# Optimization experiments

Hardware: AMD Instinct MI355X
Metric: run time of the kernel (lower is better)

## Reference

```python
import jax, jax.numpy as jnp
import numpy as np

T, N, D = 64, 40, 4
H, R, K = 256, 64, 2
E = N * (N - 1)


def _xavier(key, shape):
    std = (2.0 / (shape[0] + shape[1])) ** 0.5
    return (std * jax.random.normal(key, shape)).astype(jnp.float32)


def setup_inputs() -> dict:
    ks = iter(jax.random.split(jax.random.key(0), 40))
    send, recv = np.where(np.ones((N, N)) - np.eye(N))  # fully-connected directed graph, E = N*(N-1)
    p = {}
    p['inputs'] = jax.random.normal(next(ks), (1, T, N, D), dtype=jnp.float32)
    p['node_masks'] = jnp.ones((1, T, N), dtype=jnp.float32)
    p['send_edges'] = jnp.asarray(send, dtype=jnp.int32)
    p['recv_edges'] = jnp.asarray(recv, dtype=jnp.int32)
    for name, nin in (('mlp1', D), ('mlp2', 2 * H), ('mlp3', H), ('mlp4', 3 * H)):
        p[name + '_W1'] = _xavier(next(ks), (H, nin))
        p[name + '_b1'] = jnp.full((H,), 0.1, jnp.float32)
        p[name + '_W2'] = _xavier(next(ks), (H, H))
        p[name + '_b2'] = jnp.full((H,), 0.1, jnp.float32)
    s = float(1.0 / np.sqrt(R))
    for nm in ('fwd', 'rev'):
        p[nm + '_Wih'] = jax.random.uniform(next(ks), (4 * R, H), jnp.float32, -s, s)
        p[nm + '_Whh'] = jax.random.uniform(next(ks), (4 * R, R), jnp.float32, -s, s)
        p[nm + '_bih'] = jnp.zeros((4 * R,), jnp.float32)
        p[nm + '_bhh'] = jnp.zeros((4 * R,), jnp.float32)
    p['enc_W'] = _xavier(next(ks), (K, 2 * R))
    p['enc_b'] = jnp.full((K,), 0.1, jnp.float32)
    p['prior_W'] = _xavier(next(ks), (K, R))
    p['prior_b'] = jnp.full((K,), 0.1, jnp.float32)
    return p


def _mlp(x, W1, b1, W2, b2):
    # RefNRIMLP in eval mode with no_bn=True: elu(fc2(elu(fc1(x))))
    return jax.nn.elu(jax.nn.elu(x @ W1.T + b1) @ W2.T + b2)


def _lstm(xs, Wih, Whh, bih, bhh):
    # xs: [T, E, H] -> hidden states [T, E, R]; PyTorch LSTM gate order i, f, g, o
    def step(carry, xt):
        h, c = carry
        g = xt @ Wih.T + bih + h @ Whh.T + bhh
        i, f, gg, o = jnp.split(g, 4, axis=-1)
        c = jax.nn.sigmoid(f) * c + jax.nn.sigmoid(i) * jnp.tanh(gg)
        h = jax.nn.sigmoid(o) * jnp.tanh(c)
        return (h, c), h
    Rh = Whh.shape[1]
    init = (jnp.zeros((xs.shape[1], Rh), xs.dtype), jnp.zeros((xs.shape[1], Rh), xs.dtype))
    _, hs = jax.lax.scan(step, init, xs)
    return hs


def _encode(inputs, send, recv,
            m1W1, m1b1, m1W2, m1b2, m2W1, m2b1, m2W2, m2b2,
            m3W1, m3b1, m3W2, m3b2, m4W1, m4b1, m4W2, m4b2,
            fWih, fWhh, fbih, fbhh, rWih, rWhh, rbih, rbhh,
            encW, encb, priW, prib):
    x = inputs[0]                                                  # [T, N, D]
    h = _mlp(x, m1W1, m1b1, m1W2, m1b2)                            # [T, N, H]
    e = jnp.concatenate([h[:, send], h[:, recv]], axis=-1)         # node2edge gather [T, E, 2H]
    e = _mlp(e, m2W1, m2b1, m2W2, m2b2)                            # [T, E, H]
    skip = e
    n = jnp.zeros((x.shape[0], x.shape[1], e.shape[-1]), e.dtype)
    n = n.at[:, recv].add(e)                                       # edge2node scatter-add (index_add_)
    n = _mlp(n, m3W1, m3b1, m3W2, m3b2)                            # [T, N, H]
    e = jnp.concatenate([n[:, send], n[:, recv], skip], axis=-1)   # [T, E, 3H]
    e = _mlp(e, m4W1, m4b1, m4W2, m4b2)                            # per-edge features over time [T, E, H]
    fwd_h = _lstm(e, fWih, fWhh, fbih, fbhh)                       # [T, E, R]
    rev_h = _lstm(e[::-1], rWih, rWhh, rbih, rbhh)[::-1]           # [T, E, R]
    prior = fwd_h @ priW.T + prib                                  # [T, E, K]
    enc = jnp.concatenate([fwd_h, rev_h], axis=-1) @ encW.T + encb # [T, E, K]
    return jnp.concatenate([prior, enc], axis=-1)                  # [T, E, 2K]


def reference(inputs, node_masks, send_edges, recv_edges,
              mlp1_W1, mlp1_b1, mlp1_W2, mlp1_b2,
              mlp2_W1, mlp2_b1, mlp2_W2, mlp2_b2,
              mlp3_W1, mlp3_b1, mlp3_W2, mlp3_b2,
              mlp4_W1, mlp4_b1, mlp4_W2, mlp4_b2,
              fwd_Wih, fwd_Whh, fwd_bih, fwd_bhh,
              rev_Wih, rev_Whh, rev_bih, rev_bhh,
              enc_W, enc_b, prior_W, prior_b):
    del node_masks  # all nodes present -> static fully-connected graph each step
    return _encode(inputs, send_edges, recv_edges,
                   mlp1_W1, mlp1_b1, mlp1_W2, mlp1_b2,
                   mlp2_W1, mlp2_b1, mlp2_W2, mlp2_b2,
                   mlp3_W1, mlp3_b1, mlp3_W2, mlp3_b2,
                   mlp4_W1, mlp4_b1, mlp4_W2, mlp4_b2,
                   fwd_Wih, fwd_Whh, fwd_bih, fwd_bhh,
                   rev_Wih, rev_Whh, rev_bih, rev_bhh,
                   enc_W, enc_b, prior_W, prior_b)
```

## Files before the change

### kernel.cpp

```cpp
#include <hip/hip_runtime.h>
#include <math.h>

#define T_ 64
#define N_ 40
#define D_ 4
#define H_ 256
#define R_ 64
#define E_ 1560
#define TE_ (T_*E_)
#define TN_ (T_*N_)

typedef unsigned short us;
typedef short short8 __attribute__((ext_vector_type(8)));
typedef float f32x4 __attribute__((ext_vector_type(4)));

__device__ __forceinline__ float elu_f(float x){ return x > 0.f ? x : (__expf(x) - 1.f); }
__device__ __forceinline__ float sig_f(float x){ return 1.f/(1.f+__expf(-x)); }
__device__ __forceinline__ float tanh_f(float x){ return 2.f/(1.f+__expf(-2.f*x)) - 1.f; }
__device__ __forceinline__ float dot4(float4 a, float4 b){ return a.x*b.x + a.y*b.y + a.z*b.z + a.w*b.w; }

__device__ __forceinline__ float bf2f(us u){ return __uint_as_float(((unsigned int)u) << 16); }
__device__ __forceinline__ us f2bf(float f){
    unsigned int u = __float_as_uint(f);
    u += 0x7FFFu + ((u >> 16) & 1u);
    return (us)(u >> 16);
}
__device__ __forceinline__ float4 ld4f(const float* p){ return *(const float4*)p; }
__device__ __forceinline__ float4 ld4f(const us* p){
    ushort4 v = *(const ushort4*)p;
    return make_float4(bf2f(v.x), bf2f(v.y), bf2f(v.z), bf2f(v.w));
}
__device__ __forceinline__ void st4f(float* p, float4 v){ *(float4*)p = v; }
__device__ __forceinline__ void st4f(us* p, float4 v){
    ushort4 o; o.x = f2bf(v.x); o.y = f2bf(v.y); o.z = f2bf(v.z); o.w = f2bf(v.w);
    *(ushort4*)p = o;
}

__device__ __forceinline__ void gld16(void* lds, const void* g){
    __builtin_amdgcn_global_load_lds((const __attribute__((address_space(1))) unsigned int*)g,
                                     (__attribute__((address_space(3))) unsigned int*)lds,
                                     16, 0, 0);
}

__device__ __forceinline__ void wsplit1(const float* W, us* hi, us* lo, int i){
    const float w = W[i];
    const us h = f2bf(w);
    hi[i] = h;
    lo[i] = f2bf(w - bf2f(h));
}

__device__ __forceinline__ void wsplitF(const float* __restrict__ W, int stride, int colOff,
                                        us* hi, us* lo, int i){
    const int jj   = i & 7;
    const int lane = (i >> 3) & 63;
    const int mt   = (i >> 9) & 1;
    const int k    = (i >> 10) & 7;
    const int fh   = i >> 13;
    const int R = fh * 32 + mt * 16 + (lane & 15);
    const int K = k * 32 + (lane >> 4) * 8 + jj;
    const float w = W[(size_t)R * stride + colOff + K];
    const us h = f2bf(w);
    hi[i] = h;
    lo[i] = f2bf(w - bf2f(h));
}

__global__ __launch_bounds__(256)
void wsplit_all(const float* __restrict__ s0, us* h0, us* l0,
                const float* __restrict__ s1, us* h1, us* l1,
                const float* __restrict__ s2, us* h2, us* l2,
                const float* __restrict__ s3, us* h3, us* l3,
                const float* __restrict__ s4, us* h4, us* l4,
                const float* __restrict__ s5, us* h5, us* l5,
                const float* __restrict__ s6, us* h6, us* l6)
{
    int i = blockIdx.x * 256 + threadIdx.x;
    if (i < 65536) { wsplitF(s0, 256,   0, h0, l0, i); return; } i -= 65536;
    if (i < 65536) { wsplitF(s1, 768, 512, h1, l1, i); return; } i -= 65536;
    if (i < 65536) { wsplitF(s2, 256,   0, h2, l2, i); return; } i -= 65536;
    if (i < 65536) { wsplitF(s3, 256,   0, h3, l3, i); return; } i -= 65536;
    if (i < 65536) { wsplitF(s4, 256,   0, h4, l4, i); return; } i -= 65536;
    if (i < 16384) { wsplit1(s5, h5, l5, i); return; } i -= 16384;
    wsplit1(s6, h6, l6, i);
}

__global__ __launch_bounds__(256)
void mlp1_kernel(const float* __restrict__ x,
                 const float* __restrict__ W1, const float* __restrict__ b1,
                 const float* __restrict__ W2, const float* __restrict__ b2,
                 us* __restrict__ hout)
{
    __shared__ float xs[8][4];
    __shared__ float h1[8][256];
    const int tid = threadIdx.x;
    const int r0  = blockIdx.x * 8;

    if (tid < 32) xs[tid >> 2][tid & 3] = x[r0 * 4 + tid];
    __syncthreads();

    const float4 w1 = *(const float4*)&W1[tid * 4];
    const float bb1 = b1[tid];
    #pragma unroll
    for (int row = 0; row < 8; ++row) {
        float v = bb1 + xs[row][0]*w1.x + xs[row][1]*w1.y + xs[row][2]*w1.z + xs[row][3]*w1.w;
        h1[row][tid] = elu_f(v);
    }
    __syncthreads();

    float acc[8];
    const float bb2 = b2[tid];
    #pragma unroll
    for (int row = 0; row < 8; ++row) acc[row] = bb2;
    const float* w2row = W2 + (size_t)tid * 256;
    for (int k4 = 0; k4 < 64; ++k4) {
        const float4 w = *(const float4*)&w2row[k4 * 4];
        #pragma unroll
        for (int row = 0; row < 8; ++row) {
            const float4 hh = *(const float4*)&h1[row][k4 * 4];
            acc[row] += dot4(hh, w);
        }
    }
    #pragma unroll
    for (int row = 0; row < 8; ++row)
        hout[(size_t)(r0 + row) * 256 + tid] = f2bf(elu_f(acc[row]));
}

__global__ __launch_bounds__(256)
void node_proj(const us* __restrict__ A, const float* __restrict__ W,
               int wstride, float* __restrict__ P)
{
    __shared__ float As[16][64];
    __shared__ float Ws[16][64];

    const int tid  = threadIdx.x;
    const int am   = tid >> 2;
    const int gm   = blockIdx.x * 64 + am;
    const int part = blockIdx.y >> 2;
    const int wq   = blockIdx.y & 3;

    const us* aptr = A + (size_t)gm * 256;
    const float* wptr = W + (size_t)(wq * 64 + am) * wstride + part * 256;

    const int tx = tid & 15, ty = tid >> 4;
    float acc[4][4] = {};

    for (int k0 = 0; k0 < 256; k0 += 16) {
        const float4 a4 = ld4f(aptr + k0 + (tid & 3) * 4);
        const float4 w4 = *(const float4*)(wptr + k0 + (tid & 3) * 4);

        __syncthreads();
        const int ak = (tid & 3) * 4;
        As[ak+0][am] = a4.x; As[ak+1][am] = a4.y; As[ak+2][am] = a4.z; As[ak+3][am] = a4.w;
        Ws[ak+0][am] = w4.x; Ws[ak+1][am] = w4.y; Ws[ak+2][am] = w4.z; Ws[ak+3][am] = w4.w;
        __syncthreads();

        #pragma unroll
        for (int kq = 0; kq < 16; ++kq) {
            const float4 av = *(const float4*)&As[kq][ty * 4];
            const float4 wv = *(const float4*)&Ws[kq][tx * 4];
            const float a_[4] = {av.x, av.y, av.z, av.w};
            const float w_[4] = {wv.x, wv.y, wv.z, wv.w};
            #pragma unroll
            for (int i = 0; i < 4; ++i)
                #pragma unroll
                for (int j = 0; j < 4; ++j)
                    acc[i][j] += a_[i] * w_[j];
        }
    }

    const int gn = part * 256 + wq * 64 + tx * 4;
    #pragma unroll
    for (int i = 0; i < 4; ++i) {
        const int row = blockIdx.x * 64 + ty * 4 + i;
        float4 o;
        o.x = acc[i][0]; o.y = acc[i][1]; o.z = acc[i][2]; o.w = acc[i][3];
        *(float4*)(P + (size_t)row * 512 + gn) = o;
    }
}

#define VM0   0x3F70

#define GEMM_CORE64(WHp, WLp)                                                            \
    {                                                                                    \
        const us* wbh = (WHp) + w * 8192 + lane * 8;                                     \
        const us* wbl = (WLp) + w * 8192 + lane * 8;                                     \
        _Pragma("unroll")                                                                \
        for (int k = 0; k < 8; ++k) {                                                    \
            short8 wh[2], wl[2], ef[4];                                                  \
            _Pragma("unroll")                                                            \
            for (int mt = 0; mt < 2; ++mt) {                                             \
                wh[mt] = *(const short8*)(wbh + (k * 2 + mt) * 512);                     \
                wl[mt] = *(const short8*)(wbl + (k * 2 + mt) * 512);                     \
            }                                                                            \
            _Pragma("unroll")                                                            \
            for (int nt = 0; nt < 4; ++nt)                                               \
                ef[nt] = *(const short8*)(AG + k * 4096 + nt * 1024 + ml * 64 + qs16);   \
            __builtin_amdgcn_s_setprio(1);                                               \
            _Pragma("unroll")                                                            \
            for (int nt = 0; nt < 4; ++nt)                                               \
                _Pragma("unroll")                                                        \
                for (int mt = 0; mt < 2; ++mt) {                                         \
                    acc[mt][nt] = __builtin_amdgcn_mfma_f32_16x16x32_bf16(               \
                        wh[mt], ef[nt], acc[mt][nt], 0, 0, 0);                           \
                    acc[mt][nt] = __builtin_amdgcn_mfma_f32_16x16x32_bf16(               \
                        wl[mt], ef[nt], acc[mt][nt], 0, 0, 0);                           \
                }                                                                        \
            __builtin_amdgcn_s_setprio(0);                                               \
        }                                                                                \
    }

__global__ __launch_bounds__(512, 4)
void gemm_bf(const float* __restrict__ Ptab, const float* __restrict__ b1,
             const int* __restrict__ send, const int* __restrict__ recv,
             const us* __restrict__ WH, const us* __restrict__ WL,
             const float* __restrict__ bias2, us* __restrict__ C)
{
    __shared__ char AG[32768];

    const int tid = threadIdx.x, lane = tid & 63, w = tid >> 6;
    const int ml = lane & 15, q = lane >> 4;
    const int qs16 = (q ^ ((ml >> 1) & 3)) * 16;
    const int bx = blockIdx.x;

    {
        int srw[4], rrw[4];
        #pragma unroll
        for (int nt = 0; nt < 4; ++nt) {
            const int row = bx * 64 + nt * 16 + ml;
            const int t = row / E_;
            const int e = row - t * E_;
            srw[nt] = t * N_ + send[e];
            rrw[nt] = t * N_ + recv[e];
        }
        #pragma unroll
        for (int mt = 0; mt < 2; ++mt) {
            const int col = w * 32 + mt * 16 + q * 4;
            const float4 bb = *(const float4*)(b1 + col);
            const int of = w * 4096 + ml * 64 + (((mt * 2 + (q >> 1)) ^ ((ml >> 1) & 3)) * 16) + (q & 1) * 8;
            #pragma unroll
            for (int nt = 0; nt < 4; ++nt) {
                const float4 a = *(const float4*)(Ptab + (size_t)srw[nt] * 512 + col);
                const float4 b = *(const float4*)(Ptab + (size_t)rrw[nt] * 512 + 256 + col);
                float4 v;
                v.x = elu_f(a.x + b.x + bb.x);
                v.y = elu_f(a.y + b.y + bb.y);
                v.z = elu_f(a.z + b.z + bb.z);
                v.w = elu_f(a.w + b.w + bb.w);
                ushort4 o; o.x = f2bf(v.x); o.y = f2bf(v.y); o.z = f2bf(v.z); o.w = f2bf(v.w);
                *(ushort4*)(AG + of + nt * 1024) = o;
            }
        }
    }
    __syncthreads();

    f32x4 acc[2][4];
    #pragma unroll
    for (int mt = 0; mt < 2; ++mt)
        #pragma unroll
        for (int nt = 0; nt < 4; ++nt) acc[mt][nt] = (f32x4){0.f,0.f,0.f,0.f};

    GEMM_CORE64(WH, WL)

    #pragma unroll
    for (int mt = 0; mt < 2; ++mt) {
        const int col = w * 32 + mt * 16 + q * 4;
        const float4 bb = *(const float4*)(bias2 + col);
        #pragma unroll
        for (int nt = 0; nt < 4; ++nt) {
            const int row = bx * 64 + nt * 16 + ml;
            float4 v;
            v.x = elu_f(acc[mt][nt][0] + bb.x); v.y = elu_f(acc[mt][nt][1] + bb.y);
            v.z = elu_f(acc[mt][nt][2] + bb.z); v.w = elu_f(acc[mt][nt][3] + bb.w);
            ushort4 o; o.x = f2bf(v.x); o.y = f2bf(v.y); o.z = f2bf(v.z); o.w = f2bf(v.w);
            *(ushort4*)(C + (size_t)row * 256 + col) = o;
        }
    }
}

__global__ __launch_bounds__(512, 4)
void fused_m4(const us* __restrict__ Askip,
              const us* __restrict__ w4aH, const us* __restrict__ w4aL, const float* __restrict__ m4b1,
              const us* __restrict__ w4bH, const us* __restrict__ w4bL, const float* __restrict__ m4b2,
              const us* __restrict__ wfiH, const us* __restrict__ wfiL,
              const float* __restrict__ fbih, const float* __restrict__ fbhh,
              const us* __restrict__ wriH, const us* __restrict__ wriL,
              const float* __restrict__ rbih, const float* __restrict__ rbhh,
              const float* __restrict__ Ptab, const int* __restrict__ send, const int* __restrict__ recv,
              us* __restrict__ Gf, us* __restrict__ Gr)
{
    __shared__ char AG[32768];

    const int tid = threadIdx.x, lane = tid & 63, w = tid >> 6;
    const int ml = lane & 15, q = lane >> 4;
    const int lr = lane >> 2;
    const int cofs = (((lane & 3) ^ ((lane >> 3) & 3)) * 8);
    const int qs16 = (q ^ ((ml >> 1) & 3)) * 16;
    const int bx = blockIdx.x;

    int gtOf[2];
    #pragma unroll
    for (int mt = 0; mt < 2; ++mt)
        gtOf[mt] = w * 4096 + ml * 64 + (((mt * 2 + (q >> 1)) ^ ((ml >> 1) & 3)) * 16) + (q & 1) * 8;

    f32x4 acc[2][4];

    #pragma unroll
    for (int g = 0; g < 4; ++g)
        gld16(AG + w * 4096 + g * 1024,
              Askip + (size_t)(bx * 64 + g * 16 + lr) * 256 + w * 32 + cofs);
    __builtin_amdgcn_s_waitcnt(VM0);
    __syncthreads();

    ushort4 r16[2][4];

    #pragma unroll
    for (int mt = 0; mt < 2; ++mt)
        #pragma unroll
        for (int nt = 0; nt < 4; ++nt) acc[mt][nt] = (f32x4){0.f,0.f,0.f,0.f};
    GEMM_CORE64(w4aH, w4aL)
    {
        int srw[4], rrw[4];
        #pragma unroll
        for (int nt = 0; nt < 4; ++nt) {
            const int row = bx * 64 + nt * 16 + ml;
            const int t = row / E_;
            const int e = row - t * E_;
            srw[nt] = t * N_ + send[e];
            rrw[nt] = t * N_ + recv[e];
        }
        #pragma unroll
        for (int mt = 0; mt < 2; ++mt) {
            const int col = w * 32 + mt * 16 + q * 4;
            const float4 bb = *(const float4*)(m4b1 + col);
            #pragma unroll
            for (int nt = 0; nt < 4; ++nt) {
                float4 v;
                v.x = acc[mt][nt][0] + bb.x; v.y = acc[mt][nt][1] + bb.y;
                v.z = acc[mt][nt][2] + bb.z; v.w = acc[mt][nt][3] + bb.w;
                const float4 pS = *(const float4*)(Ptab + (size_t)srw[nt] * 512 + col);
                const float4 pR = *(const float4*)(Ptab + (size_t)rrw[nt] * 512 + 256 + col);
                v.x += pS.x + pR.x; v.y += pS.y + pR.y;
                v.z += pS.z + pR.z; v.w += pS.w + pR.w;
                v.x = elu_f(v.x); v.y = elu_f(v.y); v.z = elu_f(v.z); v.w = elu_f(v.w);
                ushort4 o; o.x = f2bf(v.x); o.y = f2bf(v.y); o.z = f2bf(v.z); o.w = f2bf(v.w);
                r16[mt][nt] = o;
            }
        }
    }
    __syncthreads();
    #pragma unroll
    for (int mt = 0; mt < 2; ++mt)
        #pragma unroll
        for (int nt = 0; nt < 4; ++nt)
            *(ushort4*)(AG + gtOf[mt] + nt * 1024) = r16[mt][nt];
    __syncthreads();

    #pragma unroll
    for (int mt = 0; mt < 2; ++mt)
        #pragma unroll
        for (int nt = 0; nt < 4; ++nt) acc[mt][nt] = (f32x4){0.f,0.f,0.f,0.f};
    GEMM_CORE64(w4bH, w4bL)
    #pragma unroll
    for (int mt = 0; mt < 2; ++mt) {
        const int col = w * 32 + mt * 16 + q * 4;
        const float4 bb = *(const float4*)(m4b2 + col);
        #pragma unroll
        for (int nt = 0; nt < 4; ++nt) {
            float4 v;
            v.x = elu_f(acc[mt][nt][0] + bb.x); v.y = elu_f(acc[mt][nt][1] + bb.y);
            v.z = elu_f(acc[mt][nt][2] + bb.z); v.w = elu_f(acc[mt][nt][3] + bb.w);
            ushort4 o; o.x = f2bf(v.x); o.y = f2bf(v.y); o.z = f2bf(v.z); o.w = f2bf(v.w);
            r16[mt][nt] = o;
        }
    }
    __syncthreads();
    #pragma unroll
    for (int mt = 0; mt < 2; ++mt)
        #pragma unroll
        for (int nt = 0; nt < 4; ++nt)
            *(ushort4*)(AG + gtOf[mt] + nt * 1024) = r16[mt][nt];
    __syncthreads();

    #pragma unroll
    for (int mt = 0; mt < 2; ++mt)
        #pragma unroll
        for (int nt = 0; nt < 4; ++nt) acc[mt][nt] = (f32x4){0.f,0.f,0.f,0.f};
    GEMM_CORE64(wfiH, wfiL)
    #pragma unroll
    for (int mt = 0; mt < 2; ++mt) {
        const int col = w * 32 + mt * 16 + q * 4;
        float4 bb = *(const float4*)(fbih + col);
        const float4 b2 = *(const float4*)(fbhh + col);
        bb.x += b2.x; bb.y += b2.y; bb.z += b2.z; bb.w += b2.w;
        #pragma unroll
        for (int nt = 0; nt < 4; ++nt) {
            const int row = bx * 64 + nt * 16 + ml;
            float4 v;
            v.x = acc[mt][nt][0] + bb.x; v.y = acc[mt][nt][1] + bb.y;
            v.z = acc[mt][nt][2] + bb.z; v.w = acc[mt][nt][3] + bb.w;
            ushort4 o; o.x = f2bf(v.x); o.y = f2bf(v.y); o.z = f2bf(v.z); o.w = f2bf(v.w);
            *(ushort4*)(Gf + (size_t)row * 256 + col) = o;
        }
    }

    #pragma unroll
    for (int mt = 0; mt < 2; ++mt)
        #pragma unroll
        for (int nt = 0; nt < 4; ++nt) acc[mt][nt] = (f32x4){0.f,0.f,0.f,0.f};
    GEMM_CORE64(wriH, wriL)
    #pragma unroll
    for (int mt = 0; mt < 2; ++mt) {
        const int col = w * 32 + mt * 16 + q * 4;
        float4 bb = *(const float4*)(rbih + col);
        const float4 b2 = *(const float4*)(rbhh + col);
        bb.x += b2.x; bb.y += b2.y; bb.z += b2.z; bb.w += b2.w;
        #pragma unroll
        for (int nt = 0; nt < 4; ++nt) {
            const int row = bx * 64 + nt * 16 + ml;
            float4 v;
            v.x = acc[mt][nt][0] + bb.x; v.y = acc[mt][nt][1] + bb.y;
            v.z = acc[mt][nt][2] + bb.z; v.w = acc[mt][nt][3] + bb.w;
            ushort4 o; o.x = f2bf(v.x); o.y = f2bf(v.y); o.z = f2bf(v.z); o.w = f2bf(v.w);
            *(ushort4*)(Gr + (size_t)row * 256 + col) = o;
        }
    }
}

template<bool DOELU, typename TA, typename TC>
__global__ __launch_bounds__(256)
void gemm_nt(const TA* __restrict__ A, const float* __restrict__ W,
             const float* __restrict__ bias1,
             TC* __restrict__ C, int M, int Kdim)
{
    __shared__ float As[16][64];
    __shared__ float Ws[16][64];

    const int tid = threadIdx.x;
    const int am  = tid >> 2;
    const int ak  = (tid & 3) * 4;
    const int gm  = blockIdx.x * 64 + am;

    const TA* aptr0 = A + (size_t)gm * Kdim;
    const float* wptr = W + (size_t)(blockIdx.y * 64 + am) * Kdim;

    const int tx = tid & 15, ty = tid >> 4;
    float acc[4][4] = {};

    for (int k0 = 0; k0 < Kdim; k0 += 16) {
        const float4 a4 = ld4f(aptr0 + k0 + ak);
        const float4 w4 = *(const float4*)(wptr + k0 + (tid & 3) * 4);

        __syncthreads();
        As[ak+0][am] = a4.x; As[ak+1][am] = a4.y; As[ak+2][am] = a4.z; As[ak+3][am] = a4.w;
        const int wk = (tid & 3) * 4;
        Ws[wk+0][am] = w4.x; Ws[wk+1][am] = w4.y; Ws[wk+2][am] = w4.z; Ws[wk+3][am] = w4.w;
        __syncthreads();

        #pragma unroll
        for (int kq = 0; kq < 16; ++kq) {
            const float4 av = *(const float4*)&As[kq][ty * 4];
            const float4 wv = *(const float4*)&Ws[kq][tx * 4];
            const float a_[4] = {av.x, av.y, av.z, av.w};
            const float w_[4] = {wv.x, wv.y, wv.z, wv.w};
            #pragma unroll
            for (int i = 0; i < 4; ++i)
                #pragma unroll
                for (int j = 0; j < 4; ++j)
                    acc[i][j] += a_[i] * w_[j];
        }
    }

    const int gn = blockIdx.y * 64 + tx * 4;
    const float4 bb = *(const float4*)&bias1[gn];
    #pragma unroll
    for (int i = 0; i < 4; ++i) {
        const int row = blockIdx.x * 64 + ty * 4 + i;
        float4 o;
        o.x = acc[i][0] + bb.x; o.y = acc[i][1] + bb.y;
        o.z = acc[i][2] + bb.z; o.w = acc[i][3] + bb.w;
        if (DOELU) { o.x = elu_f(o.x); o.y = elu_f(o.y); o.z = elu_f(o.z); o.w = elu_f(o.w); }
        st4f(C + (size_t)row * 256 + gn, o);
    }
}

__global__ __launch_bounds__(256)
void aggregate_kernel(const us* __restrict__ eSkip, const int* __restrict__ recv,
                      float* __restrict__ nAgg)
{
    const int t = blockIdx.x / N_;
    const int j = blockIdx.x - t * N_;
    const int c = threadIdx.x;
    const us* basep = eSkip + (size_t)t * E_ * H_ + c;
    float acc = 0.f;
    #pragma unroll
    for (int s = 0; s < N_; ++s) {
        if (s == j) continue;
        const int e = s * (N_ - 1) + (j < s ? j : j - 1);
        acc += bf2f(basep[(size_t)e * H_]);
    }
    nAgg[(size_t)blockIdx.x * H_ + c] = acc;
}

__global__ __launch_bounds__(256)
void lstm_mfma(const us* __restrict__ Gf, const us* __restrict__ Gr,
               const us* __restrict__ fWhhH, const us* __restrict__ fWhhL,
               const us* __restrict__ rWhhH, const us* __restrict__ rWhhL,
               float* __restrict__ hsF, float* __restrict__ hsR)
{
    const int NBD = (E_ + 15) / 16;
    const bool revd = (int)blockIdx.x >= NBD;
    const int blk = revd ? (int)blockIdx.x - NBD : (int)blockIdx.x;
    const int e0 = blk * 16;
    const us* G  = revd ? Gr : Gf;
    const us* WH = revd ? rWhhH : fWhhH;
    const us* WL = revd ? rWhhL : fWhhL;
    float* hs    = revd ? hsR : hsF;

    const int tid  = threadIdx.x;
    const int lane = tid & 63;
    const int w    = tid >> 6;
    const int ml   = lane & 15;
    const int q    = lane >> 4;

    __shared__ us hHi[2][16][72];
    __shared__ us hLo[2][16][72];

    short8 wfh[4][2], wfl[4][2];
    #pragma unroll
    for (int mt = 0; mt < 4; ++mt) {
        const int row = mt * 64 + w * 16 + ml;
        #pragma unroll
        for (int ks = 0; ks < 2; ++ks) {
            wfh[mt][ks] = *(const short8*)(WH + (size_t)row * 64 + ks * 32 + q * 8);
            wfl[mt][ks] = *(const short8*)(WL + (size_t)row * 64 + ks * 32 + q * 8);
        }
    }

    for (int i = tid; i < 16 * 72; i += 256) { (&hHi[0][0][0])[i] = 0; (&hLo[0][0][0])[i] = 0; }

    const int eMF = min(e0 + ml, E_ - 1);
    const bool wr = (e0 + ml) < E_;
    const int gOfs = w * 16 + q * 4;
    float4 cst = make_float4(0.f, 0.f, 0.f, 0.f);

    ushort4 gcur[4], gnxt[4];
    {
        const int tt0 = revd ? (T_ - 1) : 0;
        const us* gp = G + ((size_t)tt0 * E_ + eMF) * 256 + gOfs;
        #pragma unroll
        for (int mt = 0; mt < 4; ++mt) gcur[mt] = *(const ushort4*)(gp + mt * 64);
    }
    __syncthreads();

    for (int s = 0; s < T_; ++s) {
        const int tt = revd ? (T_ - 1 - s) : s;
        {
            const int sn = (s + 1 < T_) ? s + 1 : s;
            const int tn = revd ? (T_ - 1 - sn) : sn;
            const us* gp = G + ((size_t)tn * E_ + eMF) * 256 + gOfs;
            #pragma unroll
            for (int mt = 0; mt < 4; ++mt) gnxt[mt] = *(const ushort4*)(gp + mt * 64);
        }
        const int rb = s & 1, wb = rb ^ 1;
        short8 bh[2], bl[2];
        #pragma unroll
        for (int ks = 0; ks < 2; ++ks) {
            bh[ks] = *(const short8*)(&hHi[rb][ml][ks * 32 + q * 8]);
            bl[ks] = *(const short8*)(&hLo[rb][ml][ks * 32 + q * 8]);
        }
        f32x4 acc[4];
        #pragma unroll
        for (int mt = 0; mt < 4; ++mt) {
            acc[mt][0] = bf2f(gcur[mt].x); acc[mt][1] = bf2f(gcur[mt].y);
            acc[mt][2] = bf2f(gcur[mt].z); acc[mt][3] = bf2f(gcur[mt].w);
            #pragma unroll
            for (int ks = 0; ks < 2; ++ks) {
                acc[mt] = __builtin_amdgcn_mfma_f32_16x16x32_bf16(wfh[mt][ks], bh[ks], acc[mt], 0, 0, 0);
                acc[mt] = __builtin_amdgcn_mfma_f32_16x16x32_bf16(wfh[mt][ks], bl[ks], acc[mt], 0, 0, 0);
                acc[mt] = __builtin_amdgcn_mfma_f32_16x16x32_bf16(wfl[mt][ks], bh[ks], acc[mt], 0, 0, 0);
            }
        }
        float4 hv;
        cst.x = sig_f(acc[1][0])*cst.x + sig_f(acc[0][0])*tanh_f(acc[2][0]); hv.x = sig_f(acc[3][0])*tanh_f(cst.x);
        cst.y = sig_f(acc[1][1])*cst.y + sig_f(acc[0][1])*tanh_f(acc[2][1]); hv.y = sig_f(acc[3][1])*tanh_f(cst.y);
        cst.z = sig_f(acc[1][2])*cst.z + sig_f(acc[0][2])*tanh_f(acc[2][2]); hv.z = sig_f(acc[3][2])*tanh_f(cst.z);
        cst.w = sig_f(acc[1][3])*cst.w + sig_f(acc[0][3])*tanh_f(acc[2][3]); hv.w = sig_f(acc[3][3])*tanh_f(cst.w);
        ushort4 hh4, hl4;
        hh4.x = f2bf(hv.x); hl4.x = f2bf(hv.x - bf2f(hh4.x));
        hh4.y = f2bf(hv.y); hl4.y = f2bf(hv.y - bf2f(hh4.y));
        hh4.z = f2bf(hv.z); hl4.z = f2bf(hv.z - bf2f(hh4.z));
        hh4.w = f2bf(hv.w); hl4.w = f2bf(hv.w - bf2f(hh4.w));
        *(ushort4*)(&hHi[wb][ml][gOfs]) = hh4;
        *(ushort4*)(&hLo[wb][ml][gOfs]) = hl4;
        if (wr)
            *(float4*)(&hs[((size_t)tt * E_ + e0 + ml) * 64 + gOfs]) = hv;
        __syncthreads();
        #pragma unroll
        for (int mt = 0; mt < 4; ++mt) gcur[mt] = gnxt[mt];
    }
}

__global__ __launch_bounds__(256)
void out_kernel(const float* __restrict__ hsF, const float* __restrict__ hsR,
                const float* __restrict__ priW, const float* __restrict__ prib,
                const float* __restrict__ encW, const float* __restrict__ encb,
                float* __restrict__ out)
{
    const int idx = blockIdx.x * 256 + threadIdx.x;
    const float* f = hsF + (size_t)idx * 64;
    const float* r = hsR + (size_t)idx * 64;
    float p0 = prib[0], p1 = prib[1], q0 = encb[0], q1 = encb[1];
    #pragma unroll
    for (int k4 = 0; k4 < 16; ++k4) {
        const float4 fv = *(const float4*)(f + k4 * 4);
        const float4 rv = *(const float4*)(r + k4 * 4);
        p0 += dot4(fv, *(const float4*)(priW + k4 * 4));
        p1 += dot4(fv, *(const float4*)(priW + 64 + k4 * 4));
        q0 += dot4(fv, *(const float4*)(encW + k4 * 4))
            + dot4(rv, *(const float4*)(encW + 64 + k4 * 4));
        q1 += dot4(fv, *(const float4*)(encW + 128 + k4 * 4))
            + dot4(rv, *(const float4*)(encW + 192 + k4 * 4));
    }
    float4 o; o.x = p0; o.y = p1; o.z = q0; o.w = q1;
    *(float4*)(out + (size_t)idx * 4) = o;
}

extern "C" void kernel_launch(void* const* d_in, const int* in_sizes, int n_in,
                              void* d_out, int out_size, void* d_ws, size_t ws_size,
                              hipStream_t stream)
{
    const float* x    = (const float*)d_in[0];
    const int*   send = (const int*)d_in[2];
    const int*   recv = (const int*)d_in[3];
    const float* m1W1 = (const float*)d_in[4];  const float* m1b1 = (const float*)d_in[5];
    const float* m1W2 = (const float*)d_in[6];  const float* m1b2 = (const float*)d_in[7];
    const float* m2W1 = (const float*)d_in[8];  const float* m2b1 = (const float*)d_in[9];
    const float* m2W2 = (const float*)d_in[10]; const float* m2b2 = (const float*)d_in[11];
    const float* m3W1 = (const float*)d_in[12]; const float* m3b1 = (const float*)d_in[13];
    const float* m3W2 = (const float*)d_in[14]; const float* m3b2 = (const float*)d_in[15];
    const float* m4W1 = (const float*)d_in[16]; const float* m4b1 = (const float*)d_in[17];
    const float* m4W2 = (const float*)d_in[18]; const float* m4b2 = (const float*)d_in[19];
    const float* fWih = (const float*)d_in[20]; const float* fWhh = (const float*)d_in[21];
    const float* fbih = (const float*)d_in[22]; const float* fbhh = (const float*)d_in[23];
    const float* rWih = (const float*)d_in[24]; const float* rWhh = (const float*)d_in[25];
    const float* rbih = (const float*)d_in[26]; const float* rbhh = (const float*)d_in[27];
    const float* encW = (const float*)d_in[28]; const float* encb = (const float*)d_in[29];
    const float* priW = (const float*)d_in[30]; const float* prib = (const float*)d_in[31];

    const size_t SZN  = (size_t)TN_ * H_;
    const size_t SZE  = (size_t)TE_ * H_;
    float* n_agg = (float*)d_ws;
    float* m3t   = n_agg + SZN;
    float* Ptab  = (float*)d_ws;
    us* h16      = (us*)(m3t + SZN);
    us* n3       = h16 + SZN;
    us* w2bH = n3  + SZN;          us* w2bL = w2bH + 65536;
    us* w4aH = w2bL + 65536;       us* w4aL = w4aH + 65536;
    us* w4bH = w4aL + 65536;       us* w4bL = w4bH + 65536;
    us* wfiH = w4bL + 65536;       us* wfiL = wfiH + 65536;
    us* wriH = wfiL + 65536;       us* wriL = wriH + 65536;
    us* whfH = wriL + 65536;       us* whfL = whfH + 16384;
    us* whrH = whfL + 16384;       us* whrL = whrH + 16384;
    us* bufA16 = whrL + 16384;
    us* bufB16 = bufA16 + SZE;
    us* bufC16 = bufB16 + SZE;
    float* hsF = (float*)bufC16;
    float* hsR = hsF + (size_t)TE_ * R_;
    const size_t needed = ((size_t)(bufC16 + SZE) - (size_t)d_ws);
    if (ws_size < needed) return;

    const dim3 gN(TN_ / 64, 4), gNP(TN_ / 64, 8);

    wsplit_all<<<1408, 256, 0, stream>>>(m2W2, w2bH, w2bL,
                                         m4W1, w4aH, w4aL,
                                         m4W2, w4bH, w4bL,
                                         fWih, wfiH, wfiL, rWih, wriH, wriL,
                                         fWhh, whfH, whfL, rWhh, whrH, whrL);

    mlp1_kernel<<<TN_ / 8, 256, 0, stream>>>(x, m1W1, m1b1, m1W2, m1b2, h16);
    node_proj<<<gNP, 256, 0, stream>>>(h16, m2W1, 512, Ptab);
    gemm_bf<<<TE_ / 64, 512, 0, stream>>>(Ptab, m2b1, send, recv, w2bH, w2bL, m2b2, bufB16);
    aggregate_kernel<<<TN_, 256, 0, stream>>>(bufB16, recv, n_agg);
    gemm_nt<true, float, float><<<gN, 256, 0, stream>>>(n_agg, m3W1, m3b1, m3t, TN_, 256);
    gemm_nt<true, float, us><<<gN, 256, 0, stream>>>(m3t, m3W2, m3b2, n3, TN_, 256);
    node_proj<<<gNP, 256, 0, stream>>>(n3, m4W1, 768, Ptab);
    fused_m4<<<TE_ / 64, 512, 0, stream>>>(bufB16,
                                           w4aH, w4aL, m4b1,
                                           w4bH, w4bL, m4b2,
                                           wfiH, wfiL, fbih, fbhh,
                                           wriH, wriL, rbih, rbhh,
                                           Ptab, send, recv, bufA16, bufB16);
    lstm_mfma<<<2 * ((E_ + 15) / 16), 256, 0, stream>>>(bufA16, bufB16, whfH, whfL, whrH, whrL, hsF, hsR);
    out_kernel<<<TE_ / 256, 256, 0, stream>>>(hsF, hsR, priW, prib, encW, encb, (float*)d_out);
}
```

Baseline: 505.3 us.

## Process 128 edge rows per block in fused_m4 to reuse weight fragments

fused_m4 now handles two 64-row tiles per block, staging both in a doubled 64KB LDS buffer. Each weight fragment loaded from global memory feeds MFMAs for both tiles, halving weight traffic per row across all four chained GEMMs. In exchange, accumulator registers double, launch bounds drop to 2 blocks per CU, and the grid halves to 780 blocks, which lowers occupancy and parallelism.

```diff
diff --git a/kernel.cpp b/kernel.cpp
--- a/kernel.cpp
+++ b/kernel.cpp
@@ -208,6 +208,58 @@
         }                                                                                \
     }
 
+#define CORE2P(WHp, WLp)                                                                 \
+    {                                                                                    \
+        const us* wbh = (WHp) + w * 8192 + lane * 8;                                     \
+        const us* wbl = (WLp) + w * 8192 + lane * 8;                                     \
+        _Pragma("unroll")                                                                \
+        for (int k = 0; k < 8; ++k) {                                                    \
+            short8 wh[2], wl[2], ef[4];                                                  \
+            _Pragma("unroll")                                                            \
+            for (int mt = 0; mt < 2; ++mt) {                                             \
+                wh[mt] = *(const short8*)(wbh + (k * 2 + mt) * 512);                     \
+                wl[mt] = *(const short8*)(wbl + (k * 2 + mt) * 512);                     \
+            }                                                                            \
+            _Pragma("unroll")                                                            \
+            for (int nt = 0; nt < 4; ++nt)                                               \
+                ef[nt] = *(const short8*)(AG + k * 4096 + nt * 1024 + ml * 64 + qs16);   \
+            __builtin_amdgcn_s_setprio(1);                                               \
+            _Pragma("unroll")                                                            \
+            for (int nt = 0; nt < 4; ++nt)                                               \
+                _Pragma("unroll")                                                        \
+                for (int mt = 0; mt < 2; ++mt) {                                         \
+                    acc0[mt][nt] = __builtin_amdgcn_mfma_f32_16x16x32_bf16(              \
+                        wh[mt], ef[nt], acc0[mt][nt], 0, 0, 0);                          \
+                    acc0[mt][nt] = __builtin_amdgcn_mfma_f32_16x16x32_bf16(              \
+                        wl[mt], ef[nt], acc0[mt][nt], 0, 0, 0);                          \
+                }                                                                        \
+            __builtin_amdgcn_s_setprio(0);                                               \
+            _Pragma("unroll")                                                            \
+            for (int nt = 0; nt < 4; ++nt)                                               \
+                ef[nt] = *(const short8*)(AG + 32768 + k * 4096 + nt * 1024 + ml * 64 + qs16); \
+            __builtin_amdgcn_s_setprio(1);                                               \
+            _Pragma("unroll")                                                            \
+            for (int nt = 0; nt < 4; ++nt)                                               \
+                _Pragma("unroll")                                                        \
+                for (int mt = 0; mt < 2; ++mt) {                                         \
+                    acc1[mt][nt] = __builtin_amdgcn_mfma_f32_16x16x32_bf16(              \
+                        wh[mt], ef[nt], acc1[mt][nt], 0, 0, 0);                          \
+                    acc1[mt][nt] = __builtin_amdgcn_mfma_f32_16x16x32_bf16(              \
+                        wl[mt], ef[nt], acc1[mt][nt], 0, 0, 0);                          \
+                }                                                                        \
+            __builtin_amdgcn_s_setprio(0);                                               \
+        }                                                                                \
+    }
+
+#define ZERO2                                                                            \
+    _Pragma("unroll")                                                                    \
+    for (int mt = 0; mt < 2; ++mt)                                                       \
+        _Pragma("unroll")                                                                \
+        for (int nt = 0; nt < 4; ++nt) {                                                 \
+            acc0[mt][nt] = (f32x4){0.f,0.f,0.f,0.f};                                     \
+            acc1[mt][nt] = (f32x4){0.f,0.f,0.f,0.f};                                     \
+        }
+
 __global__ __launch_bounds__(512, 4)
 void gemm_bf(const float* __restrict__ Ptab, const float* __restrict__ b1,
              const int* __restrict__ send, const int* __restrict__ recv,
@@ -276,7 +328,7 @@
     }
 }
 
-__global__ __launch_bounds__(512, 4)
+__global__ __launch_bounds__(512, 2)
 void fused_m4(const us* __restrict__ Askip,
               const us* __restrict__ w4aH, const us* __restrict__ w4aL, const float* __restrict__ m4b1,
               const us* __restrict__ w4bH, const us* __restrict__ w4bL, const float* __restrict__ m4b2,
@@ -287,7 +339,7 @@
               const float* __restrict__ Ptab, const int* __restrict__ send, const int* __restrict__ recv,
               us* __restrict__ Gf, us* __restrict__ Gr)
 {
-    __shared__ char AG[32768];
+    __shared__ char AG[65536];
 
     const int tid = threadIdx.x, lane = tid & 63, w = tid >> 6;
     const int ml = lane & 15, q = lane >> 4;
@@ -301,64 +353,74 @@
     for (int mt = 0; mt < 2; ++mt)
         gtOf[mt] = w * 4096 + ml * 64 + (((mt * 2 + (q >> 1)) ^ ((ml >> 1) & 3)) * 16) + (q & 1) * 8;
 
-    f32x4 acc[2][4];
-
-    #pragma unroll
-    for (int g = 0; g < 4; ++g)
-        gld16(AG + w * 4096 + g * 1024,
-              Askip + (size_t)(bx * 64 + g * 16 + lr) * 256 + w * 32 + cofs);
+    f32x4 acc0[2][4], acc1[2][4];
+
+    #pragma unroll
+    for (int p = 0; p < 2; ++p)
+        #pragma unroll
+        for (int g = 0; g < 4; ++g)
+            gld16(AG + p * 32768 + w * 4096 + g * 1024,
+                  Askip + (size_t)(bx * 128 + p * 64 + g * 16 + lr) * 256 + w * 32 + cofs);
     __builtin_amdgcn_s_waitcnt(VM0);
     __syncthreads();
 
-    ushort4 r16[2][4];
-
-    #pragma unroll
-    for (int mt = 0; mt < 2; ++mt)
-        #pragma unroll
-        for (int nt = 0; nt < 4; ++nt) acc[mt][nt] = (f32x4){0.f,0.f,0.f,0.f};
-    GEMM_CORE64(w4aH, w4aL)
+    ushort4 r16a[2][4], r16b[2][4];
+
+    ZERO2
+    CORE2P(w4aH, w4aL)
     {
-        int srw[4], rrw[4];
-        #pragma unroll
-        for (int nt = 0; nt < 4; ++nt) {
-            const int row = bx * 64 + nt * 16 + ml;
-            const int t = row / E_;
-            const int e = row - t * E_;
-            srw[nt] = t * N_ + send[e];
-            rrw[nt] = t * N_ + recv[e];
-        }
         #pragma unroll
         for (int mt = 0; mt < 2; ++mt) {
             const int col = w * 32 + mt * 16 + q * 4;
             const float4 bb = *(const float4*)(m4b1 + col);
             #pragma unroll
             for (int nt = 0; nt < 4; ++nt) {
+                const int row = bx * 128 + nt * 16 + ml;
+                const int t = row / E_;
+                const int e = row - t * E_;
+                const int sr = t * N_ + send[e], rr = t * N_ + recv[e];
                 float4 v;
-                v.x = acc[mt][nt][0] + bb.x; v.y = acc[mt][nt][1] + bb.y;
-                v.z = acc[mt][nt][2] + bb.z; v.w = acc[mt][nt][3] + bb.w;
-                const float4 pS = *(const float4*)(Ptab + (size_t)srw[nt] * 512 + col);
-                const float4 pR = *(const float4*)(Ptab + (size_t)rrw[nt] * 512 + 256 + col);
+                v.x = acc0[mt][nt][0] + bb.x; v.y = acc0[mt][nt][1] + bb.y;
+                v.z = acc0[mt][nt][2] + bb.z; v.w = acc0[mt][nt][3] + bb.w;
+                const float4 pS = *(const float4*)(Ptab + (size_t)sr * 512 + col);
+                const float4 pR = *(const float4*)(Ptab + (size_t)rr * 512 + 256 + col);
                 v.x += pS.x + pR.x; v.y += pS.y + pR.y;
                 v.z += pS.z + pR.z; v.w += pS.w + pR.w;
                 v.x = elu_f(v.x); v.y = elu_f(v.y); v.z = elu_f(v.z); v.w = elu_f(v.w);
                 ushort4 o; o.x = f2bf(v.x); o.y = f2bf(v.y); o.z = f2bf(v.z); o.w = f2bf(v.w);
-                r16[mt][nt] = o;
+                r16a[mt][nt] = o;
             }
+            #pragma unroll
+            for (int nt = 0; nt < 4; ++nt) {
+                const int row = bx * 128 + 64 + nt * 16 + ml;
+                const int t = row / E_;
+                const int e = row - t * E_;
+                const int sr = t * N_ + send[e], rr = t * N_ + recv[e];
+                float4 v;
+                v.x = acc1[mt][nt][0] + bb.x; v.y = acc1[mt][nt][1] + bb.y;
+                v.z = acc1[mt][nt][2] + bb.z; v.w = acc1[mt][nt][3] + bb.w;
+                const float4 pS = *(const float4*)(Ptab + (size_t)sr * 512 + col);
+                const float4 pR = *(const float4*)(Ptab + (size_t)rr * 512 + 256 + col);
+                v.x += pS.x + pR.x; v.y += pS.y + pR.y;
+                v.z += pS.z + pR.z; v.w += pS.w + pR.w;
+                v.x = elu_f(v.x); v.y = elu_f(v.y); v.z = elu_f(v.z); v.w = elu_f(v.w);
+                ushort4 o; o.x = f2bf(v.x); o.y = f2bf(v.y); o.z = f2bf(v.z); o.w = f2bf(v.w);
+                r16b[mt][nt] = o;
+            }
         }
     }
     __syncthreads();
     #pragma unroll
     for (int mt = 0; mt < 2; ++mt)
         #pragma unroll
-        for (int nt = 0; nt < 4; ++nt)
-            *(ushort4*)(AG + gtOf[mt] + nt * 1024) = r16[mt][nt];
-    __syncthreads();
-
-    #pragma unroll
-    for (int mt = 0; mt < 2; ++mt)
-        #pragma unroll
-        for (int nt = 0; nt < 4; ++nt) acc[mt][nt] = (f32x4){0.f,0.f,0.f,0.f};
-    GEMM_CORE64(w4bH, w4bL)
+        for (int nt = 0; nt < 4; ++nt) {
+            *(ushort4*)(AG + gtOf[mt] + nt * 1024) = r16a[mt][nt];
+            *(ushort4*)(AG + 32768 + gtOf[mt] + nt * 1024) = r16b[mt][nt];
+        }
+    __syncthreads();
+
+    ZERO2
+    CORE2P(w4bH, w4bL)
     #pragma unroll
     for (int mt = 0; mt < 2; ++mt) {
         const int col = w * 32 + mt * 16 + q * 4;
@@ -366,25 +428,28 @@
         #pragma unroll
         for (int nt = 0; nt < 4; ++nt) {
             float4 v;
-            v.x = elu_f(acc[mt][nt][0] + bb.x); v.y = elu_f(acc[mt][nt][1] + bb.y);
-            v.z = elu_f(acc[mt][nt][2] + bb.z); v.w = elu_f(acc[mt][nt][3] + bb.w);
+            v.x = elu_f(acc0[mt][nt][0] + bb.x); v.y = elu_f(acc0[mt][nt][1] + bb.y);
+            v.z = elu_f(acc0[mt][nt][2] + bb.z); v.w = elu_f(acc0[mt][nt][3] + bb.w);
             ushort4 o; o.x = f2bf(v.x); o.y = f2bf(v.y); o.z = f2bf(v.z); o.w = f2bf(v.w);
-            r16[mt][nt] = o;
+            r16a[mt][nt] = o;
+            v.x = elu_f(acc1[mt][nt][0] + bb.x); v.y = elu_f(acc1[mt][nt][1] + bb.y);
+            v.z = elu_f(acc1[mt][nt][2] + bb.z); v.w = elu_f(acc1[mt][nt][3] + bb.w);
+            ushort4 o2; o2.x = f2bf(v.x); o2.y = f2bf(v.y); o2.z = f2bf(v.z); o2.w = f2bf(v.w);
+            r16b[mt][nt] = o2;
         }
     }
     __syncthreads();
     #pragma unroll
     for (int mt = 0; mt < 2; ++mt)
         #pragma unroll
-        for (int nt = 0; nt < 4; ++nt)
-            *(ushort4*)(AG + gtOf[mt] + nt * 1024) = r16[mt][nt];
-    __syncthreads();
-
-    #pragma unroll
-    for (int mt = 0; mt < 2; ++mt)
-        #pragma unroll
-        for (int nt = 0; nt < 4; ++nt) acc[mt][nt] = (f32x4){0.f,0.f,0.f,0.f};
-    GEMM_CORE64(wfiH, wfiL)
+        for (int nt = 0; nt < 4; ++nt) {
+            *(ushort4*)(AG + gtOf[mt] + nt * 1024) = r16a[mt][nt];
+            *(ushort4*)(AG + 32768 + gtOf[mt] + nt * 1024) = r16b[mt][nt];
+        }
+    __syncthreads();
+
+    ZERO2
+    CORE2P(wfiH, wfiL)
     #pragma unroll
     for (int mt = 0; mt < 2; ++mt) {
         const int col = w * 32 + mt * 16 + q * 4;
@@ -393,20 +458,22 @@
         bb.x += b2.x; bb.y += b2.y; bb.z += b2.z; bb.w += b2.w;
         #pragma unroll
         for (int nt = 0; nt < 4; ++nt) {
-            const int row = bx * 64 + nt * 16 + ml;
+            const int row0 = bx * 128 + nt * 16 + ml;
             float4 v;
-            v.x = acc[mt][nt][0] + bb.x; v.y = acc[mt][nt][1] + bb.y;
-            v.z = acc[mt][nt][2] + bb.z; v.w = acc[mt][nt][3] + bb.w;
+            v.x = acc0[mt][nt][0] + bb.x; v.y = acc0[mt][nt][1] + bb.y;
+            v.z = acc0[mt][nt][2] + bb.z; v.w = acc0[mt][nt][3] + bb.w;
             ushort4 o; o.x = f2bf(v.x); o.y = f2bf(v.y); o.z = f2bf(v.z); o.w = f2bf(v.w);
-            *(ushort4*)(Gf + (size_t)row * 256 + col) = o;
-        }
-    }
-
-    #pragma unroll
-    for (int mt = 0; mt < 2; ++mt)
-        #pragma unroll
-        for (int nt = 0; nt < 4; ++nt) acc[mt][nt] = (f32x4){0.f,0.f,0.f,0.f};
-    GEMM_CORE64(wriH, wriL)
+            *(ushort4*)(Gf + (size_t)row0 * 256 + col) = o;
+            const int row1 = row0 + 64;
+            v.x = acc1[mt][nt][0] + bb.x; v.y = acc1[mt][nt][1] + bb.y;
+            v.z = acc1[mt][nt][2] + bb.z; v.w = acc1[mt][nt][3] + bb.w;
+            ushort4 o2; o2.x = f2bf(v.x); o2.y = f2bf(v.y); o2.z = f2bf(v.z); o2.w = f2bf(v.w);
+            *(ushort4*)(Gf + (size_t)row1 * 256 + col) = o2;
+        }
+    }
+
+    ZERO2
+    CORE2P(wriH, wriL)
     #pragma unroll
     for (int mt = 0; mt < 2; ++mt) {
         const int col = w * 32 + mt * 16 + q * 4;
@@ -415,12 +482,17 @@
         bb.x += b2.x; bb.y += b2.y; bb.z += b2.z; bb.w += b2.w;
         #pragma unroll
         for (int nt = 0; nt < 4; ++nt) {
-            const int row = bx * 64 + nt * 16 + ml;
+            const int row0 = bx * 128 + nt * 16 + ml;
             float4 v;
-            v.x = acc[mt][nt][0] + bb.x; v.y = acc[mt][nt][1] + bb.y;
-            v.z = acc[mt][nt][2] + bb.z; v.w = acc[mt][nt][3] + bb.w;
+            v.x = acc0[mt][nt][0] + bb.x; v.y = acc0[mt][nt][1] + bb.y;
+            v.z = acc0[mt][nt][2] + bb.z; v.w = acc0[mt][nt][3] + bb.w;
             ushort4 o; o.x = f2bf(v.x); o.y = f2bf(v.y); o.z = f2bf(v.z); o.w = f2bf(v.w);
-            *(ushort4*)(Gr + (size_t)row * 256 + col) = o;
+            *(ushort4*)(Gr + (size_t)row0 * 256 + col) = o;
+            const int row1 = row0 + 64;
+            v.x = acc1[mt][nt][0] + bb.x; v.y = acc1[mt][nt][1] + bb.y;
+            v.z = acc1[mt][nt][2] + bb.z; v.w = acc1[mt][nt][3] + bb.w;
+            ushort4 o2; o2.x = f2bf(v.x); o2.y = f2bf(v.y); o2.z = f2bf(v.z); o2.w = f2bf(v.w);
+            *(ushort4*)(Gr + (size_t)row1 * 256 + col) = o2;
         }
     }
 }
@@ -683,12 +755,12 @@
     gemm_nt<true, float, float><<<gN, 256, 0, stream>>>(n_agg, m3W1, m3b1, m3t, TN_, 256);
     gemm_nt<true, float, us><<<gN, 256, 0, stream>>>(m3t, m3W2, m3b2, n3, TN_, 256);
     node_proj<<<gNP, 256, 0, stream>>>(n3, m4W1, 768, Ptab);
-    fused_m4<<<TE_ / 64, 512, 0, stream>>>(bufB16,
-                                           w4aH, w4aL, m4b1,
-                                           w4bH, w4bL, m4b2,
-                                           wfiH, wfiL, fbih, fbhh,
-                                           wriH, wriL, rbih, rbhh,
-                                           Ptab, send, recv, bufA16, bufB16);
+    fused_m4<<<TE_ / 128, 512, 0, stream>>>(bufB16,
+                                            w4aH, w4aL, m4b1,
+                                            w4bH, w4bL, m4b2,
+                                            wfiH, wfiL, fbih, fbhh,
+                                            wriH, wriL, rbih, rbhh,
+                                            Ptab, send, recv, bufA16, bufB16);
     lstm_mfma<<<2 * ((E_ + 15) / 16), 256, 0, stream>>>(bufA16, bufB16, whfH, whfL, whrH, whrL, hsF, hsR);
     out_kernel<<<TE_ / 256, 256, 0, stream>>>(hsF, hsR, priW, prib, encW, encb, (float*)d_out);
 }
```

After: 510.3 us. Within noise of the previous version (+1.0%).
